# Kernel tuning notes

Hardware: AMD Instinct MI355X
Metric: run time of the kernel (lower is better)

## Reference

```python
import jax, jax.numpy as jnp
import numpy as np
from jax import lax

N_QUBITS = 4
N_QLAYERS = 2
C64 = jnp.complex64
PAIRS = [(i, j) for i in range(N_QUBITS) for j in range(i + 1, N_QUBITS)]  # 6 entangling pairs
CNOT = jnp.array([[1, 0, 0, 0], [0, 1, 0, 0], [0, 0, 0, 1], [0, 0, 1, 0]], dtype=C64)


def _rx(t):
    c = jnp.cos(t / 2).astype(C64)
    s = (-1j * jnp.sin(t / 2)).astype(C64)
    return jnp.stack([jnp.stack([c, s]), jnp.stack([s, c])])


def _ry(t):
    c = jnp.cos(t / 2).astype(C64)
    s = jnp.sin(t / 2).astype(C64)
    return jnp.stack([jnp.stack([c, -s]), jnp.stack([s, c])])


def _rz(t):
    e = jnp.exp(-1j * t.astype(C64) / 2)
    z = jnp.zeros_like(e)
    return jnp.stack([jnp.stack([e, z]), jnp.stack([z, jnp.conj(e)])])


def _apply_1q(state, M, w):
    # state: (B,2,2,2,2); M: (2,2) shared or (B,2,2) per-sample
    s = jnp.moveaxis(state, 1 + w, -1)
    if M.ndim == 2:
        s = jnp.einsum('b...j,ij->b...i', s, M)
    else:
        s = jnp.einsum('b...j,bij->b...i', s, M)
    return jnp.moveaxis(s, -1, 1 + w)


def _apply_2q(state, M4, c, t):
    # M4: (4,4) acting on (wire c, wire t)
    s = jnp.moveaxis(state, (1 + c, 1 + t), (-2, -1))
    sh = s.shape
    s = s.reshape(sh[:-2] + (4,))
    s = jnp.einsum('b...j,ij->b...i', s, M4)
    s = s.reshape(sh)
    return jnp.moveaxis(s, (-2, -1), (1 + c, 1 + t))


def _quantum_batched(angles, q_params):
    # angles: (B, 4) classical outputs; encoding is RY(angles*pi)
    B = angles.shape[0]
    state = jnp.zeros((B, 16), C64).at[:, 0].set(1.0).reshape(B, 2, 2, 2, 2)
    theta = angles * jnp.float32(np.pi)
    c = jnp.cos(theta / 2).astype(C64)  # (B,4)
    s = jnp.sin(theta / 2).astype(C64)
    for w in range(N_QUBITS):
        M = jnp.stack([jnp.stack([c[:, w], -s[:, w]], -1),
                       jnp.stack([s[:, w], c[:, w]], -1)], -2)  # (B,2,2)
        state = _apply_1q(state, M, w)
    per_layer = 3 * N_QUBITS + len(PAIRS)  # 18
    for l in range(N_QLAYERS):
        start = l * per_layer
        rot = q_params[start:start + 3 * N_QUBITS].reshape(N_QUBITS, 3)
        ent = q_params[start + 3 * N_QUBITS:start + per_layer]
        for q in range(N_QUBITS):
            M = _rz(rot[q, 2]) @ _ry(rot[q, 1]) @ _rx(rot[q, 0])
            state = _apply_1q(state, M, q)
        for k, (i, j) in enumerate(PAIRS):
            M4 = jnp.kron(jnp.eye(2, dtype=C64), _rz(ent[k])) @ CNOT  # CNOT then RZ on target
            state = _apply_2q(state, M4, i, j)
    probs = jnp.abs(state) ** 2  # (B,2,2,2,2)
    signs = jnp.array([1.0, -1.0], jnp.float32)
    zs = []
    for w in range(N_QUBITS):
        pw = jnp.moveaxis(probs, 1 + w, -1).reshape(B, -1, 2)
        zs.append((pw.sum(1) * signs).sum(-1))
    return jnp.stack(zs, -1)  # (B,4) PauliZ expvals


def _conv(x, w, b):
    y = lax.conv_general_dilated(x, w, (1, 1), ((1, 1), (1, 1)),
                                 dimension_numbers=('NCHW', 'OIHW', 'NCHW'))
    return y + b[None, :, None, None]


def _pool(x):
    return lax.reduce_window(x, -jnp.inf, lax.max, (1, 1, 2, 2), (1, 1, 2, 2), 'VALID')


def setup_inputs() -> dict:
    key = jax.random.key(0)
    ks = jax.random.split(key, 10)
    B = 4096
    return {
        'x': jax.random.normal(ks[0], (B, 1, 28, 28), jnp.float32),
        'conv1_w': jax.random.normal(ks[1], (16, 1, 3, 3), jnp.float32) * 0.1,
        'conv1_b': jax.random.normal(ks[2], (16,), jnp.float32) * 0.1,
        'conv2_w': jax.random.normal(ks[3], (32, 16, 3, 3), jnp.float32) * 0.05,
        'conv2_b': jax.random.normal(ks[4], (32,), jnp.float32) * 0.1,
        'dense_w': jax.random.normal(ks[5], (4, 1568), jnp.float32) * 0.02,
        'dense_b': jax.random.normal(ks[6], (4,), jnp.float32) * 0.1,
        'q_params': jax.random.normal(ks[7], (36,), jnp.float32) * 0.1,
        'post_w': jax.random.normal(ks[8], (10, 4), jnp.float32) * 0.5,
        'post_b': jax.random.normal(ks[9], (10,), jnp.float32) * 0.1,
    }


def reference(x, conv1_w, conv1_b, conv2_w, conv2_b, dense_w, dense_b, q_params, post_w, post_b):
    h = jax.nn.relu(_conv(x, conv1_w, conv1_b))
    h = _pool(h)
    h = jax.nn.relu(_conv(h, conv2_w, conv2_b))
    h = _pool(h)  # (B,32,7,7)
    h = h.reshape(h.shape[0], 32 * 7 * 7)
    # dropout is identity in eval mode
    angles = h @ dense_w.T + dense_b  # (B,4)
    z = _quantum_batched(angles, q_params)  # (B,4)
    return z @ post_w.T + post_b  # (B,10)
```

## Files before the change

kernel.cpp:

```cpp
#include <hip/hip_runtime.h>

#define PI_F 3.14159265358979323846f

typedef _Float16 half2v __attribute__((ext_vector_type(2)));
typedef _Float16 half4v __attribute__((ext_vector_type(4)));
typedef _Float16 half8v __attribute__((ext_vector_type(8)));
typedef float f32x4 __attribute__((ext_vector_type(4)));

struct C2 { float x, y; };
__device__ __forceinline__ C2 cmul(C2 a, C2 b) {
    return C2{a.x * b.x - a.y * b.y, a.x * b.y + a.y * b.x};
}

__device__ __forceinline__ void gate1(float& re, float& im, int l, int w,
                                      C2 m00, C2 m01, C2 m10, C2 m11) {
    int mask = 1 << (3 - w);
    float pre = __shfl_xor(re, mask, 64);
    float pim = __shfl_xor(im, mask, 64);
    bool b = (l & mask) != 0;
    C2 d = b ? m11 : m00;
    C2 o = b ? m10 : m01;
    float nre = d.x * re - d.y * im + o.x * pre - o.y * pim;
    float nim = d.x * im + d.y * re + o.x * pim + o.y * pre;
    re = nre; im = nim;
}

__global__ __launch_bounds__(256, 4) void qnn_one(
    const float* __restrict__ xg,
    const float* __restrict__ w1g, const float* __restrict__ b1g,
    const float* __restrict__ w2g, const float* __restrict__ b2g,
    const float* __restrict__ dwg, const float* __restrict__ dbg,
    const float* __restrict__ qpg,
    const float* __restrict__ pwg, const float* __restrict__ pbg,
    float* __restrict__ out, int Btot)
{
    const int b4 = blockIdx.x << 2;
    const int t = threadIdx.x;
    const int lane = t & 63;
    const int wv = __builtin_amdgcn_readfirstlane(t >> 6);
    const int kq = lane >> 4;
    const int lm = lane & 15;

    __shared__ __align__(16) unsigned xhl[1200];
    __shared__ __align__(16) float4 w2f[640];
    __shared__ __align__(16) char ovl[21632];
    __shared__ __align__(16) float angp[64];
    __shared__ float grot[64];
    __shared__ float gent[24];

    float*     w2s = (float*)ovl;
    _Float16*  p1f = (_Float16*)ovl;
    float*     p2s = (float*)(ovl + 15360);

    int xoff[5];
    {
        int y = t / 40, x = t - y * 40;
        #pragma unroll
        for (int it = 0; it < 5; ++it) {
            bool ok = (t + it * 256 < 1200) && y >= 1 && y <= 28 && x >= 1 && x <= 28;
            xoff[it] = ok ? (y * 28 + x - 29) : -1;
            x += 16; y += 6; if (x >= 40) { x -= 40; y += 1; }
        }
    }

    float xr[5];
    {
        const float* xb = xg + (size_t)b4 * 784;
        #pragma unroll
        for (int it = 0; it < 5; ++it)
            xr[it] = (xoff[it] >= 0 && b4 < Btot) ? xb[xoff[it]] : 0.f;
    }

    #pragma unroll
    for (int i = 0; i < 18; ++i)
        w2s[t + i * 256] = w2g[t + i * 256];

    float dwr0[7], dwr1[7], dwr2[7], dwr3[7];
    #pragma unroll
    for (int k2 = 0; k2 < 7; ++k2) {
        int i = t + k2 * 256;
        bool ok = i < 1568;
        dwr0[k2] = ok ? dwg[i] : 0.f;
        dwr1[k2] = ok ? dwg[1568 + i] : 0.f;
        dwr2[k2] = ok ? dwg[3136 + i] : 0.f;
        dwr3[k2] = ok ? dwg[4704 + i] : 0.f;
    }

    half4v bC1 = {(_Float16)0.f, (_Float16)0.f, (_Float16)0.f, (_Float16)0.f};
    if (kq < 3) {
        #pragma unroll
        for (int j = 0; j < 3; ++j)
            bC1[j] = (_Float16)w1g[lm * 9 + kq * 3 + j];
    }
    float bias1 = b1g[lm];
    float b20 = b2g[lm], b21 = b2g[16 + lm];

    if (t < 8) {
        int layer = t >> 2, q = t & 3;
        int st = layer * 18;
        float a0 = qpg[st + 3 * q], a1 = qpg[st + 3 * q + 1], a2 = qpg[st + 3 * q + 2];
        float cx = cosf(0.5f * a0), sx = sinf(0.5f * a0);
        float cy = cosf(0.5f * a1), sy = sinf(0.5f * a1);
        float cz = cosf(0.5f * a2), sz = sinf(0.5f * a2);
        C2 T00{cy * cx,  sy * sx}, T01{-sy * cx, -cy * sx};
        C2 T10{sy * cx, -cy * sx}, T11{ cy * cx, -sy * sx};
        C2 E0{cz, -sz}, E1{cz, sz};
        C2 m00 = cmul(E0, T00), m01 = cmul(E0, T01);
        C2 m10 = cmul(E1, T10), m11 = cmul(E1, T11);
        float* gm = grot + t * 8;
        gm[0] = m00.x; gm[1] = m00.y; gm[2] = m01.x; gm[3] = m01.y;
        gm[4] = m10.x; gm[5] = m10.y; gm[6] = m11.x; gm[7] = m11.y;
    }
    if (t >= 32 && t < 44) {
        int k = t - 32;
        float e = qpg[(k / 6) * 18 + 12 + (k % 6)];
        gent[k * 2]     = cosf(0.5f * e);
        gent[k * 2 + 1] = sinf(0.5f * e);
    }

    #pragma unroll
    for (int it = 0; it < 5; ++it) {
        int j = t + it * 256;
        if (it < 4 || j < 1200) {
            float v = xr[it];
            _Float16 h = (_Float16)v;
            _Float16 lo = (_Float16)(v - (float)h);
            half2v p; p.x = h; p.y = lo;
            xhl[j] = __builtin_bit_cast(unsigned, p);
        }
    }

    __syncthreads();

    for (int e = t; e < 640; e += 256) {
        int kstep = e >> 7, rem = e & 127;
        int ntile = rem >> 6, ln = rem & 63;
        int fkq = ln >> 4, n = ln & 15;
        int oc = ntile * 16 + n;
        int pi = kstep * 2 + (fkq >> 1);
        half8v h;
        #pragma unroll
        for (int jj = 0; jj < 8; ++jj) {
            int ic = (fkq & 1) * 8 + jj;
            float v = (pi < 9) ? w2s[oc * 144 + ic * 9 + pi] : 0.f;
            h[jj] = (_Float16)v;
        }
        w2f[e] = __builtin_bit_cast(float4, h);
    }

    __syncthreads();

    {
        uint4 z4 = {0u, 0u, 0u, 0u};
        uint4* p4 = (uint4*)p1f;
        #pragma unroll
        for (int j = 0; j < 4; ++j) {
            int i = t + j * 256;
            if (i < 960) p4[i] = z4;
        }
    }
    {
        const float* xb = xg + (size_t)(b4 + 1) * 784;
        #pragma unroll
        for (int it = 0; it < 5; ++it)
            xr[it] = (xoff[it] >= 0 && b4 + 1 < Btot) ? xb[xoff[it]] : 0.f;
    }

    const int kyc = (kq < 3) ? kq : 0;
    int base_i, wa_i, X_i, c_i;
    {
        int pos1 = lm & 3, pyo = pos1 >> 1, pxo = pos1 & 1;
        int p14 = wv * 4 + (lm >> 2);
        int Y = p14 / 14, X = p14 - Y * 14;
        base_i = (2 * Y + pyo + kyc) * 40 + 2 * X + pxo;
        X_i = X;
        int q14 = wv * 4 + kq;
        int r = q14 / 14, c = q14 - r * 14;
        wa_i = ((r + 1) * 20 + (c + 1)) * 24 + lm;
        c_i = c;
    }
    const int ich = (kq & 1) * 8;
    int a2_[4], quadO_[4];
    #pragma unroll
    for (int it2 = 0; it2 < 4; ++it2) {
        int tile = wv + it2 * 4;
        int tt = (tile < 13) ? tile : 12;
        int m = tt * 16 + lm;
        int quad = m >> 2; if (quad > 48) quad = 48;
        int pos = m & 3;
        int Y = quad / 7, X = quad - Y * 7;
        int py = 2 * Y + (pos >> 1), px = 2 * X + (pos & 1);
        a2_[it2] = (py * 20 + px) * 24 + ich;
        quadO_[it2] = tile * 4 + kq;
    }
    int koff_[5];
    #pragma unroll
    for (int ks = 0; ks < 5; ++ks) {
        int pi = ks * 2 + (kq >> 1); if (pi > 8) pi = 8;
        int ky = (pi >= 6) ? 2 : ((pi >= 3) ? 1 : 0);
        int kx = pi - ky * 3;
        koff_[ks] = (ky * 20 + kx) * 24;
    }

    __syncthreads();

    for (int e = 0; e < 4; ++e) {
        {
            int base = base_i, wa = wa_i, X = X_i, c = c_i;
            for (int tile = wv; tile < 49; tile += 4) {
                unsigned u0 = xhl[base], u1 = xhl[base + 1], u2 = xhl[base + 2];
                half2v h0 = __builtin_bit_cast(half2v, u0);
                half2v h1 = __builtin_bit_cast(half2v, u1);
                half2v h2 = __builtin_bit_cast(half2v, u2);
                half4v ah = {h0.x, h1.x, h2.x, (_Float16)0.f};
                half4v al = {h0.y, h1.y, h2.y, (_Float16)0.f};
                f32x4 acc = {bias1, bias1, bias1, bias1};
                acc = __builtin_amdgcn_mfma_f32_16x16x16f16(ah, bC1, acc, 0, 0, 0);
                acc = __builtin_amdgcn_mfma_f32_16x16x16f16(al, bC1, acc, 0, 0, 0);
                float v = fmaxf(fmaxf(fmaxf(acc.x, acc.y), fmaxf(acc.z, acc.w)), 0.f);
                p1f[wa] = (_Float16)v;
                X += 2; bool wR = X >= 14; base += wR ? 136 : 84; if (wR) X -= 14;
                c += 2; bool wW = c >= 14; wa   += wW ? 672 : 528; if (wW) c -= 14;
            }
        }
        __syncthreads();

        if (e < 3) {
            #pragma unroll
            for (int it = 0; it < 5; ++it) {
                int j = t + it * 256;
                if (it < 4 || j < 1200) {
                    float v = xr[it];
                    _Float16 h = (_Float16)v;
                    _Float16 lo = (_Float16)(v - (float)h);
                    half2v p; p.x = h; p.y = lo;
                    xhl[j] = __builtin_bit_cast(unsigned, p);
                }
            }
            if (e < 2) {
                const float* xb = xg + (size_t)(b4 + e + 2) * 784;
                #pragma unroll
                for (int it = 0; it < 5; ++it)
                    xr[it] = (xoff[it] >= 0 && b4 + e + 2 < Btot) ? xb[xoff[it]] : 0.f;
            }
        }

        {
            half8v B0[5], B1[5];
            const float4* wf = w2f;
            #pragma unroll
            for (int ks = 0; ks < 5; ++ks) {
                B0[ks] = __builtin_bit_cast(half8v, wf[(ks * 2 + 0) * 64 + lane]);
                B1[ks] = __builtin_bit_cast(half8v, wf[(ks * 2 + 1) * 64 + lane]);
            }
            #pragma unroll
            for (int it2 = 0; it2 < 4; ++it2) {
                if (wv + it2 * 4 < 13) {
                    f32x4 acc0 = {b20, b20, b20, b20};
                    f32x4 acc1 = {b21, b21, b21, b21};
                    #pragma unroll
                    for (int ks = 0; ks < 5; ++ks) {
                        half8v a = *(const half8v*)(&p1f[a2_[it2] + koff_[ks]]);
                        acc0 = __builtin_amdgcn_mfma_f32_16x16x32_f16(a, B0[ks], acc0, 0, 0, 0);
                        acc1 = __builtin_amdgcn_mfma_f32_16x16x32_f16(a, B1[ks], acc1, 0, 0, 0);
                    }
                    int qO = quadO_[it2];
                    if (qO < 49) {
                        float v0 = fmaxf(fmaxf(fmaxf(acc0.x, acc0.y), fmaxf(acc0.z, acc0.w)), 0.f);
                        float v1 = fmaxf(fmaxf(fmaxf(acc1.x, acc1.y), fmaxf(acc1.z, acc1.w)), 0.f);
                        p2s[lm * 49 + qO] = v0;
                        p2s[784 + lm * 49 + qO] = v1;
                    }
                }
            }
        }
        __syncthreads();

        {
            float dp0 = 0.f, dp1 = 0.f, dp2 = 0.f, dp3 = 0.f;
            #pragma unroll
            for (int k2 = 0; k2 < 7; ++k2) {
                int i = t + k2 * 256;
                if (k2 < 6 || i < 1568) {
                    float v = p2s[i];
                    dp0 = fmaf(v, dwr0[k2], dp0);
                    dp1 = fmaf(v, dwr1[k2], dp1);
                    dp2 = fmaf(v, dwr2[k2], dp2);
                    dp3 = fmaf(v, dwr3[k2], dp3);
                }
            }
            #pragma unroll
            for (int m = 32; m >= 1; m >>= 1) {
                dp0 += __shfl_xor(dp0, m, 64);
                dp1 += __shfl_xor(dp1, m, 64);
                dp2 += __shfl_xor(dp2, m, 64);
                dp3 += __shfl_xor(dp3, m, 64);
            }
            if (lane == 0) {
                float4 dpv = {dp0, dp1, dp2, dp3};
                *(float4*)&angp[e * 16 + wv * 4] = dpv;
            }
        }
    }
    __syncthreads();

    {
        const int bi = b4 + wv;
        const float* ap = angp + wv * 16;
        float4 a0v = *(const float4*)(ap);
        float4 a1v = *(const float4*)(ap + 4);
        float4 a2v = *(const float4*)(ap + 8);
        float4 a3v = *(const float4*)(ap + 12);
        float aw[4] = {a0v.x + a1v.x + a2v.x + a3v.x + dbg[0],
                       a0v.y + a1v.y + a2v.y + a3v.y + dbg[1],
                       a0v.z + a1v.z + a2v.z + a3v.z + dbg[2],
                       a0v.w + a1v.w + a2v.w + a3v.w + dbg[3]};
        int l = lm;
        float re = (l == 0) ? 1.f : 0.f;
        float im = 0.f;
        #pragma unroll
        for (int w = 0; w < 4; ++w) {
            float th = aw[w] * (PI_F * 0.5f);
            float cth = cosf(th), sth = sinf(th);
            gate1(re, im, l, w, C2{cth, 0.f}, C2{-sth, 0.f}, C2{sth, 0.f}, C2{cth, 0.f});
        }
        #pragma unroll
        for (int layer = 0; layer < 2; ++layer) {
            #pragma unroll
            for (int q = 0; q < 4; ++q) {
                const float* gm = grot + (layer * 4 + q) * 8;
                gate1(re, im, l, q, C2{gm[0], gm[1]}, C2{gm[2], gm[3]},
                                     C2{gm[4], gm[5]}, C2{gm[6], gm[7]});
            }
            const int pi_[6] = {0, 0, 0, 1, 1, 2};
            const int pj_[6] = {1, 2, 3, 2, 3, 3};
            #pragma unroll
            for (int k = 0; k < 6; ++k) {
                int i = pi_[k], j = pj_[k];
                const float* em = gent + (layer * 6 + k) * 2;
                float ce = em[0], se = em[1];
                int maskj = 1 << (3 - j);
                float pre = __shfl_xor(re, maskj, 64);
                float pim = __shfl_xor(im, maskj, 64);
                bool ci = ((l >> (3 - i)) & 1) != 0;
                re = ci ? pre : re;
                im = ci ? pim : im;
                bool bj = (l & maskj) != 0;
                C2 ph{ce, bj ? se : -se};
                C2 rr = cmul(C2{re, im}, ph);
                re = rr.x; im = rr.y;
            }
        }
        float pr = re * re + im * im;
        float z0 = ((l >> 3) & 1) ? -pr : pr;
        float z1 = ((l >> 2) & 1) ? -pr : pr;
        float z2 = ((l >> 1) & 1) ? -pr : pr;
        float z3 = (l & 1)        ? -pr : pr;
        #pragma unroll
        for (int m = 1; m <= 8; m <<= 1) {
            z0 += __shfl_xor(z0, m, 64);
            z1 += __shfl_xor(z1, m, 64);
            z2 += __shfl_xor(z2, m, 64);
            z3 += __shfl_xor(z3, m, 64);
        }
        if (lane < 10 && bi < Btot) {
            float4 pw4 = *(const float4*)(pwg + lane * 4);
            float o = pbg[lane];
            o = fmaf(z0, pw4.x, o); o = fmaf(z1, pw4.y, o);
            o = fmaf(z2, pw4.z, o); o = fmaf(z3, pw4.w, o);
            out[(size_t)bi * 10 + lane] = o;
        }
    }
}

extern "C" void kernel_launch(void* const* d_in, const int* in_sizes, int n_in,
                              void* d_out, int out_size, void* d_ws, size_t ws_size,
                              hipStream_t stream) {
    const float* x  = (const float*)d_in[0];
    const float* w1 = (const float*)d_in[1];
    const float* b1 = (const float*)d_in[2];
    const float* w2 = (const float*)d_in[3];
    const float* b2 = (const float*)d_in[4];
    const float* dw = (const float*)d_in[5];
    const float* db = (const float*)d_in[6];
    const float* qp = (const float*)d_in[7];
    const float* pw = (const float*)d_in[8];
    const float* pb = (const float*)d_in[9];
    float* out = (float*)d_out;
    int B = in_sizes[0] / 784;
    int nb = (B + 3) >> 2;

    qnn_one<<<nb, 256, 0, stream>>>(x, w1, b1, w2, b2, dw, db, qp, pw, pb, out, B);
}
```

Before: 110.2 us.

## Process two samples per block, build conv2 weights directly from global, shrink LDS

Each block now handles two images instead of four, doubling the grid, and launch bounds are raised to allow five blocks per CU. Conv2 fp16 weight fragments are built straight from global memory, which drops the staging copy to LDS and two barriers. The padded pooled-conv1 buffer uses a narrower row stride and pooled conv2 outputs are stored as fp16, which shrinks LDS. Angle cos/sin switch to fast intrinsics. The cost is that per-block setup (weight conversion, dense-weight register loads) is amortized over fewer samples, and there is some extra precision loss.

```diff
diff --git a/kernel.cpp b/kernel.cpp
--- a/kernel.cpp
+++ b/kernel.cpp
@@ -25,7 +25,7 @@
     re = nre; im = nim;
 }
 
-__global__ __launch_bounds__(256, 4) void qnn_one(
+__global__ __launch_bounds__(256, 5) void qnn_one(
     const float* __restrict__ xg,
     const float* __restrict__ w1g, const float* __restrict__ b1g,
     const float* __restrict__ w2g, const float* __restrict__ b2g,
@@ -34,7 +34,7 @@
     const float* __restrict__ pwg, const float* __restrict__ pbg,
     float* __restrict__ out, int Btot)
 {
-    const int b4 = blockIdx.x << 2;
+    const int b2 = blockIdx.x << 1;
     const int t = threadIdx.x;
     const int lane = t & 63;
     const int wv = __builtin_amdgcn_readfirstlane(t >> 6);
@@ -43,14 +43,13 @@
 
     __shared__ __align__(16) unsigned xhl[1200];
     __shared__ __align__(16) float4 w2f[640];
-    __shared__ __align__(16) char ovl[21632];
-    __shared__ __align__(16) float angp[64];
+    __shared__ __align__(16) char ovl[15424];
+    __shared__ __align__(16) float angp[32];
     __shared__ float grot[64];
     __shared__ float gent[24];
 
-    float*     w2s = (float*)ovl;
-    _Float16*  p1f = (_Float16*)ovl;
-    float*     p2s = (float*)(ovl + 15360);
+    _Float16* p1f = (_Float16*)ovl;
+    _Float16* p2s = (_Float16*)(ovl + 12288);
 
     int xoff[5];
     {
@@ -65,15 +64,11 @@
 
     float xr[5];
     {
-        const float* xb = xg + (size_t)b4 * 784;
+        const float* xb = xg + (size_t)b2 * 784;
         #pragma unroll
         for (int it = 0; it < 5; ++it)
-            xr[it] = (xoff[it] >= 0 && b4 < Btot) ? xb[xoff[it]] : 0.f;
-    }
-
-    #pragma unroll
-    for (int i = 0; i < 18; ++i)
-        w2s[t + i * 256] = w2g[t + i * 256];
+            xr[it] = (xoff[it] >= 0 && b2 < Btot) ? xb[xoff[it]] : 0.f;
+    }
 
     float dwr0[7], dwr1[7], dwr2[7], dwr3[7];
     #pragma unroll
@@ -84,6 +79,21 @@
         dwr1[k2] = ok ? dwg[1568 + i] : 0.f;
         dwr2[k2] = ok ? dwg[3136 + i] : 0.f;
         dwr3[k2] = ok ? dwg[4704 + i] : 0.f;
+    }
+
+    for (int ee = t; ee < 640; ee += 256) {
+        int kstep = ee >> 7, rem = ee & 127;
+        int ntile = rem >> 6, ln = rem & 63;
+        int fkq = ln >> 4, n = ln & 15;
+        int oc = ntile * 16 + n;
+        int pi = kstep * 2 + (fkq >> 1);
+        bool ok = pi < 9;
+        const float* wp = w2g + oc * 144 + (fkq & 1) * 72 + (ok ? pi : 0);
+        half8v h;
+        #pragma unroll
+        for (int jj = 0; jj < 8; ++jj)
+            h[jj] = ok ? (_Float16)wp[jj * 9] : (_Float16)0.f;
+        w2f[ee] = __builtin_bit_cast(float4, h);
     }
 
     half4v bC1 = {(_Float16)0.f, (_Float16)0.f, (_Float16)0.f, (_Float16)0.f};
@@ -118,6 +128,14 @@
         gent[k * 2 + 1] = sinf(0.5f * e);
     }
 
+    {
+        uint4 z4 = {0u, 0u, 0u, 0u};
+        uint4* p4 = (uint4*)p1f;
+        #pragma unroll
+        for (int j = 0; j < 3; ++j)
+            p4[t + j * 256] = z4;
+    }
+
     #pragma unroll
     for (int it = 0; it < 5; ++it) {
         int j = t + it * 256;
@@ -129,41 +147,11 @@
             xhl[j] = __builtin_bit_cast(unsigned, p);
         }
     }
-
-    __syncthreads();
-
-    for (int e = t; e < 640; e += 256) {
-        int kstep = e >> 7, rem = e & 127;
-        int ntile = rem >> 6, ln = rem & 63;
-        int fkq = ln >> 4, n = ln & 15;
-        int oc = ntile * 16 + n;
-        int pi = kstep * 2 + (fkq >> 1);
-        half8v h;
-        #pragma unroll
-        for (int jj = 0; jj < 8; ++jj) {
-            int ic = (fkq & 1) * 8 + jj;
-            float v = (pi < 9) ? w2s[oc * 144 + ic * 9 + pi] : 0.f;
-            h[jj] = (_Float16)v;
-        }
-        w2f[e] = __builtin_bit_cast(float4, h);
-    }
-
-    __syncthreads();
-
-    {
-        uint4 z4 = {0u, 0u, 0u, 0u};
-        uint4* p4 = (uint4*)p1f;
-        #pragma unroll
-        for (int j = 0; j < 4; ++j) {
-            int i = t + j * 256;
-            if (i < 960) p4[i] = z4;
-        }
-    }
-    {
-        const float* xb = xg + (size_t)(b4 + 1) * 784;
+    {
+        const float* xb = xg + (size_t)(b2 + 1) * 784;
         #pragma unroll
         for (int it = 0; it < 5; ++it)
-            xr[it] = (xoff[it] >= 0 && b4 + 1 < Btot) ? xb[xoff[it]] : 0.f;
+            xr[it] = (xoff[it] >= 0 && b2 + 1 < Btot) ? xb[xoff[it]] : 0.f;
     }
 
     const int kyc = (kq < 3) ? kq : 0;
@@ -176,7 +164,7 @@
         X_i = X;
         int q14 = wv * 4 + kq;
         int r = q14 / 14, c = q14 - r * 14;
-        wa_i = ((r + 1) * 20 + (c + 1)) * 24 + lm;
+        wa_i = ((r + 1) * 16 + (c + 1)) * 24 + lm;
         c_i = c;
     }
     const int ich = (kq & 1) * 8;
@@ -190,7 +178,7 @@
         int pos = m & 3;
         int Y = quad / 7, X = quad - Y * 7;
         int py = 2 * Y + (pos >> 1), px = 2 * X + (pos & 1);
-        a2_[it2] = (py * 20 + px) * 24 + ich;
+        a2_[it2] = (py * 16 + px) * 24 + ich;
         quadO_[it2] = tile * 4 + kq;
     }
     int koff_[5];
@@ -199,12 +187,12 @@
         int pi = ks * 2 + (kq >> 1); if (pi > 8) pi = 8;
         int ky = (pi >= 6) ? 2 : ((pi >= 3) ? 1 : 0);
         int kx = pi - ky * 3;
-        koff_[ks] = (ky * 20 + kx) * 24;
+        koff_[ks] = (ky * 16 + kx) * 24;
     }
 
     __syncthreads();
 
-    for (int e = 0; e < 4; ++e) {
+    for (int e = 0; e < 2; ++e) {
         {
             int base = base_i, wa = wa_i, X = X_i, c = c_i;
             for (int tile = wv; tile < 49; tile += 4) {
@@ -220,12 +208,12 @@
                 float v = fmaxf(fmaxf(fmaxf(acc.x, acc.y), fmaxf(acc.z, acc.w)), 0.f);
                 p1f[wa] = (_Float16)v;
                 X += 2; bool wR = X >= 14; base += wR ? 136 : 84; if (wR) X -= 14;
-                c += 2; bool wW = c >= 14; wa   += wW ? 672 : 528; if (wW) c -= 14;
+                c += 2; bool wW = c >= 14; wa   += wW ? 480 : 432; if (wW) c -= 14;
             }
         }
         __syncthreads();
 
-        if (e < 3) {
+        if (e == 0) {
             #pragma unroll
             for (int it = 0; it < 5; ++it) {
                 int j = t + it * 256;
@@ -236,12 +224,6 @@
                     half2v p; p.x = h; p.y = lo;
                     xhl[j] = __builtin_bit_cast(unsigned, p);
                 }
-            }
-            if (e < 2) {
-                const float* xb = xg + (size_t)(b4 + e + 2) * 784;
-                #pragma unroll
-                for (int it = 0; it < 5; ++it)
-                    xr[it] = (xoff[it] >= 0 && b4 + e + 2 < Btot) ? xb[xoff[it]] : 0.f;
             }
         }
 
@@ -268,8 +250,8 @@
                     if (qO < 49) {
                         float v0 = fmaxf(fmaxf(fmaxf(acc0.x, acc0.y), fmaxf(acc0.z, acc0.w)), 0.f);
                         float v1 = fmaxf(fmaxf(fmaxf(acc1.x, acc1.y), fmaxf(acc1.z, acc1.w)), 0.f);
-                        p2s[lm * 49 + qO] = v0;
-                        p2s[784 + lm * 49 + qO] = v1;
+                        p2s[lm * 49 + qO] = (_Float16)v0;
+                        p2s[784 + lm * 49 + qO] = (_Float16)v1;
                     }
                 }
             }
@@ -282,7 +264,7 @@
             for (int k2 = 0; k2 < 7; ++k2) {
                 int i = t + k2 * 256;
                 if (k2 < 6 || i < 1568) {
-                    float v = p2s[i];
+                    float v = (float)p2s[i];
                     dp0 = fmaf(v, dwr0[k2], dp0);
                     dp1 = fmaf(v, dwr1[k2], dp1);
                     dp2 = fmaf(v, dwr2[k2], dp2);
@@ -304,8 +286,8 @@
     }
     __syncthreads();
 
-    {
-        const int bi = b4 + wv;
+    if (wv < 2) {
+        const int bi = b2 + wv;
         const float* ap = angp + wv * 16;
         float4 a0v = *(const float4*)(ap);
         float4 a1v = *(const float4*)(ap + 4);
@@ -321,7 +303,7 @@
         #pragma unroll
         for (int w = 0; w < 4; ++w) {
             float th = aw[w] * (PI_F * 0.5f);
-            float cth = cosf(th), sth = sinf(th);
+            float cth = __cosf(th), sth = __sinf(th);
             gate1(re, im, l, w, C2{cth, 0.f}, C2{-sth, 0.f}, C2{sth, 0.f}, C2{cth, 0.f});
         }
         #pragma unroll
@@ -388,7 +370,7 @@
     const float* pb = (const float*)d_in[9];
     float* out = (float*)d_out;
     int B = in_sizes[0] / 784;
-    int nb = (B + 3) >> 2;
+    int nb = (B + 1) >> 1;
 
     qnn_one<<<nb, 256, 0, stream>>>(x, w1, b1, w2, b2, dw, db, qp, pw, pb, out, B);
 }
```

New measurement: 137.8 us. 25.1% more time.
